# Optimization experiments

Hardware: AMD Instinct MI355X
Metric: run time of the kernel (lower is better)

## Reference

```python
import jax, jax.numpy as jnp
import numpy as np

B, L, D = 8, 1024, 1024  # L must equal D for the elementwise sqrt(K) divide to broadcast


def setup_inputs() -> dict:
    key = jax.random.key(0)
    ks = jax.random.split(key, 9)
    # Non-negative inputs/weights/biases so K = x @ Wk.T + bk >= 0 and sqrt(K) is finite.
    rc = jax.random.uniform(ks[0], (B, L, D), dtype=jnp.float32)
    ri = jax.random.uniform(ks[1], (B, L, D), dtype=jnp.float32)
    tc = jax.random.uniform(ks[2], (B, L, D), dtype=jnp.float32)
    scale = 0.02
    Wq = jax.random.uniform(ks[3], (D, D), dtype=jnp.float32) * scale
    Wk = jax.random.uniform(ks[4], (D, D), dtype=jnp.float32) * scale
    Wv = jax.random.uniform(ks[5], (D, D), dtype=jnp.float32) * scale
    bq = jax.random.uniform(ks[6], (D,), dtype=jnp.float32) * scale
    bk = jax.random.uniform(ks[7], (D,), dtype=jnp.float32) * scale
    bv = jax.random.uniform(ks[8], (D,), dtype=jnp.float32) * scale
    return {
        "reference_caption": rc,
        "reference_image": ri,
        "target_caption": tc,
        "Wq": Wq, "bq": bq,
        "Wk": Wk, "bk": bk,
        "Wv": Wv, "bv": bv,
    }


def reference(reference_caption, reference_image, target_caption, Wq, bq, Wk, bk, Wv, bv):
    # torch nn.Linear: y = x @ W.T + b
    Q = reference_caption @ Wq.T + bq          # [B, Lq, D]
    K = reference_image @ Wk.T + bk            # [B, Lk, D]
    V = reference_image @ Wv.T + bv            # [B, Lk, D]
    matmul_qk = jnp.einsum("bqd,bkd->bqk", Q, K)  # [B, Lq, Lk]
    # Faithful to source: elementwise divide by sqrt(K) tensor (broadcasts since Lq==Lk==D).
    scaled_logits = matmul_qk / jnp.sqrt(K)
    attention_weights = jax.nn.softmax(scaled_logits, axis=-1)
    output = jnp.einsum("bqk,bkd->bqd", attention_weights, V)
    return (output, attention_weights)
```

## Files before the change

### kernel.cpp

```cpp
#include <hip/hip_runtime.h>
#include <hip/hip_fp16.h>
#include <math.h>

typedef unsigned short u16;
typedef __attribute__((ext_vector_type(8))) _Float16 half8;
typedef __attribute__((ext_vector_type(4))) float f32x4;

#define ASLOT 4096
#define BSLOT 8192
#define SLOT  12288

__device__ __forceinline__ u16 f2h(float f){ __half h=__float2half(f); u16 r; __builtin_memcpy(&r,&h,2); return r; }
__device__ __forceinline__ float h2f(u16 u){ __half h; __builtin_memcpy(&h,&u,2); return __half2float(h); }

template<int ROWS, bool WRAP>
__device__ __forceinline__ void stage_tile(const u16* __restrict__ G, int rowbase, int ldg,
                                           int k0, u16* Ls, int tid){
#pragma unroll
    for (int p = 0; p < ROWS / 64; ++p){
        const int lin = tid + p * 256;
        const int row = lin >> 2;
        const int cg  = ((lin & 3) ^ ((row >> 1) & 3)) * 8;
        const int kk  = WRAP ? (k0 & 1023) : k0;
        const u16* g = G + (size_t)(rowbase + row) * ldg + (kk + cg);
        __builtin_amdgcn_global_load_lds(
            (__attribute__((address_space(1))) void*)g,
            (__attribute__((address_space(3))) void*)(Ls + (size_t)lin * 8), 16, 0, 0);
    }
}

template<int EPI, int BIASM, bool AWRAP, bool BWRAP>
__device__ __forceinline__ void gemm_core(
    const u16* __restrict__ A, const u16* __restrict__ B,
    const float* __restrict__ bias,
    float* __restrict__ of, u16* __restrict__ oh,
    int by, int bx, int lda, int ldb, int ldc, int K, u16* sh)
{
    const int tid  = threadIdx.x;
    const int lane = tid & 63, wv = tid >> 6;
    const int wr = (wv >> 1) * 64;
    const int wc = (wv & 1) * 128;
    const int row0 = by * 128, col0 = bx * 256;
    const int lr = lane & 15, hi = lane >> 4;
    const int co = (hi ^ ((lr >> 1) & 3)) * 8;

    f32x4 acc[4][8];
#pragma unroll
    for (int m = 0; m < 4; m++)
#pragma unroll
        for (int n = 0; n < 8; n++) acc[m][n] = (f32x4){0.f, 0.f, 0.f, 0.f};

    auto stage_set = [&](int buf, int k0){
        u16* s = sh + buf * SLOT;
        stage_tile<128, AWRAP>(A, row0, lda, k0, s, tid);
        stage_tile<256, BWRAP>(B, col0, ldb, k0, s + ASLOT, tid);
    };

    const int NIT = K >> 5;
    stage_set(0, 0);
    stage_set(1, 32);
    int bufs = 2, bufr = 0;
    for (int t = 0; t < NIT; ++t){
        if (t + 2 < NIT){ stage_set(bufs, (t + 2) << 5); bufs = (bufs + 1 == 3) ? 0 : bufs + 1; }
        const int rem = NIT - 1 - t;
        if (rem >= 2)      asm volatile("s_waitcnt vmcnt(12)" ::: "memory");
        else if (rem == 1) asm volatile("s_waitcnt vmcnt(6)" ::: "memory");
        else               asm volatile("s_waitcnt vmcnt(0)" ::: "memory");
        __builtin_amdgcn_s_barrier();
        __builtin_amdgcn_sched_barrier(0);

        const u16* s = sh + bufr * SLOT;
        bufr = (bufr + 1 == 3) ? 0 : bufr + 1;

        half8 a[4], b[8];
#pragma unroll
        for (int m = 0; m < 4; m++) a[m] = *(const half8*)&s[(wr + m * 16 + lr) * 32 + co];
#pragma unroll
        for (int n = 0; n < 8; n++) b[n] = *(const half8*)&s[ASLOT + (wc + n * 16 + lr) * 32 + co];
#pragma unroll
        for (int m = 0; m < 4; m++)
#pragma unroll
            for (int n = 0; n < 8; n++)
                acc[m][n] = __builtin_amdgcn_mfma_f32_16x16x32_f16(a[m], b[n], acc[m][n], 0, 0, 0);
        __builtin_amdgcn_sched_barrier(0);
        __builtin_amdgcn_s_barrier();
    }

#pragma unroll
    for (int m = 0; m < 4; m++) {
        const int rb = row0 + wr + m * 16 + hi * 4;
#pragma unroll
        for (int n = 0; n < 8; n++) {
            const int c = col0 + wc + n * 16 + lr;
            const float bc = (BIASM == 1) ? bias[c] : 0.f;
#pragma unroll
            for (int q = 0; q < 4; q++) {
                const int r = rb + q;
                float v = acc[m][n][q] + bc;
                if (BIASM == 2) v += bias[r];
                const size_t idx = (size_t)r * ldc + c;
                if (EPI == 0) of[idx] = v;
                else if (EPI == 1) oh[idx] = f2h(v);
                else { const u16 hh = f2h(v); oh[idx] = hh; oh[idx + 1024] = f2h(v - h2f(hh)); }
            }
        }
    }
}

__global__ __launch_bounds__(256, 2) void lin_qk_k(
    const u16* __restrict__ rc_h, const u16* __restrict__ ri_hl,
    const u16* __restrict__ Wq_h, const u16* __restrict__ Wk_h,
    const float* __restrict__ bq, const float* __restrict__ bk,
    u16* __restrict__ Q_h, u16* __restrict__ Kcat)
{
    __shared__ __align__(16) u16 sh[3 * SLOT];
    const int nwg = gridDim.x, chunk = nwg >> 3;
    const int swz = ((int)blockIdx.x & 7) * chunk + ((int)blockIdx.x >> 3);
    const int p = swz & 1, t = swz >> 1;
    if (p == 0) {
        gemm_core<1, 1, false, false>(rc_h, Wq_h, bq, nullptr, Q_h,
                                      t >> 2, t & 3, 1024, 1024, 1024, 1024, sh);
    } else {
        gemm_core<2, 1, false, true>(ri_hl, Wk_h, bk, nullptr, Kcat,
                                     t >> 2, t & 3, 2048, 1024, 2048, 2048, sh);
    }
}

__global__ __launch_bounds__(256, 2) void qkt_vt_k(
    const u16* __restrict__ Q_h, const u16* __restrict__ Kcat,
    const u16* __restrict__ ri_hl, const u16* __restrict__ Wv_h,
    const float* __restrict__ bv,
    float* __restrict__ wts, u16* __restrict__ Vt)
{
    __shared__ __align__(16) u16 sh[3 * SLOT];
    const int nwg = gridDim.x, chunk = nwg >> 3;
    const int swz = ((int)blockIdx.x & 7) * chunk + ((int)blockIdx.x >> 3);
    const int p = swz & 1, t = swz >> 1;
    if (p == 0) {
        const int z = t >> 5, rem = t & 31;
        gemm_core<0, 0, true, false>(Q_h + (size_t)z * 1048576, Kcat + (size_t)z * 1024 * 2048,
                                     nullptr, wts + (size_t)z * 1048576, nullptr,
                                     rem >> 2, rem & 3, 1024, 2048, 1024, 2048, sh);
    } else {
        gemm_core<1, 2, false, false>(Wv_h, ri_hl, bv, nullptr, Vt,
                                      t >> 5, t & 31, 1024, 2048, 8192, 1024, sh);
    }
}

__global__ __launch_bounds__(256, 2) void av_k(
    const u16* __restrict__ W_h, const u16* __restrict__ Vt, float* __restrict__ outp)
{
    __shared__ __align__(16) u16 sh[3 * SLOT];
    const int nwg = gridDim.x, chunk = nwg >> 3;
    const int wg = ((int)blockIdx.x & 7) * chunk + ((int)blockIdx.x >> 3);
    const int z = wg >> 5, rem = wg & 31;
    gemm_core<0, 0, false, false>(W_h + (size_t)z * 1048576, Vt + (size_t)z * 1024,
                                  nullptr, outp + (size_t)z * 1048576, nullptr,
                                  rem >> 2, rem & 3, 1024, 8192, 1024, 1024, sh);
}

__global__ __launch_bounds__(256)
void softmax_scale_k(float* __restrict__ W, const u16* __restrict__ Kcat, u16* __restrict__ Wh)
{
    const long row = blockIdx.x;
    float* p = W + (row << 10);
    const int tid = threadIdx.x;

    float4 v = ((const float4*)p)[tid];
    const ushort4 kh = ((const ushort4*)(Kcat + (row << 11)))[tid];
    const ushort4 kl = ((const ushort4*)(Kcat + (row << 11) + 1024))[tid];
    v.x *= rsqrtf(h2f(kh.x) + h2f(kl.x));
    v.y *= rsqrtf(h2f(kh.y) + h2f(kl.y));
    v.z *= rsqrtf(h2f(kh.z) + h2f(kl.z));
    v.w *= rsqrtf(h2f(kh.w) + h2f(kl.w));

    float m = fmaxf(fmaxf(v.x, v.y), fmaxf(v.z, v.w));
#pragma unroll
    for (int o = 32; o >= 1; o >>= 1) m = fmaxf(m, __shfl_xor(m, o));
    __shared__ float sm[4];
    const int wid = tid >> 6, lane = tid & 63;
    if (lane == 0) sm[wid] = m;
    __syncthreads();
    m = fmaxf(fmaxf(sm[0], sm[1]), fmaxf(sm[2], sm[3]));

    v.x = __expf(v.x - m); v.y = __expf(v.y - m);
    v.z = __expf(v.z - m); v.w = __expf(v.w - m);
    float s = v.x + v.y + v.z + v.w;
#pragma unroll
    for (int o = 32; o >= 1; o >>= 1) s += __shfl_xor(s, o);
    __shared__ float ss[4];
    if (lane == 0) ss[wid] = s;
    __syncthreads();
    s = ss[0] + ss[1] + ss[2] + ss[3];

    const float inv = 1.0f / s;
    v.x *= inv; v.y *= inv; v.z *= inv; v.w *= inv;
    ((float4*)p)[tid] = v;

    ushort4 ub;
    ub.x = f2h(v.x); ub.y = f2h(v.y); ub.z = f2h(v.z); ub.w = f2h(v.w);
    ((ushort4*)(Wh + (row << 10)))[tid] = ub;
}

__global__ __launch_bounds__(256)
void conv_split_k(const float4* __restrict__ x, u16* __restrict__ dst, int n4)
{
    const int i = blockIdx.x * 256 + threadIdx.x;
    if (i >= n4) return;
    const int row = i >> 8, c4 = i & 255;
    const float4 v = x[i];
    ushort4 hh, ll;
    hh.x = f2h(v.x); ll.x = f2h(v.x - h2f(hh.x));
    hh.y = f2h(v.y); ll.y = f2h(v.y - h2f(hh.y));
    hh.z = f2h(v.z); ll.z = f2h(v.z - h2f(hh.z));
    hh.w = f2h(v.w); ll.w = f2h(v.w - h2f(hh.w));
    ((ushort4*)(dst + (size_t)row * 2048))[c4] = hh;
    ((ushort4*)(dst + (size_t)row * 2048 + 1024))[c4] = ll;
}

__global__ __launch_bounds__(256)
void conv_plain4_k(const float4* __restrict__ x0, ushort4* __restrict__ y0,
                   const float4* __restrict__ x1, ushort4* __restrict__ y1,
                   const float4* __restrict__ x2, ushort4* __restrict__ y2,
                   const float4* __restrict__ x3, ushort4* __restrict__ y3)
{
    const long i = (long)blockIdx.x * 256 + threadIdx.x;
    const long n0 = 2097152, n1 = 262144;
    const float4* x; ushort4* y; long j;
    if (i < n0)            { x = x0; y = y0; j = i; }
    else if (i < n0 + n1)  { x = x1; y = y1; j = i - n0; }
    else if (i < n0 + 2*n1){ x = x2; y = y2; j = i - n0 - n1; }
    else                   { x = x3; y = y3; j = i - n0 - 2*n1; }
    const float4 v = x[j];
    ushort4 o;
    o.x = f2h(v.x); o.y = f2h(v.y); o.z = f2h(v.z); o.w = f2h(v.w);
    y[j] = o;
}

extern "C" void kernel_launch(void* const* d_in, const int* in_sizes, int n_in,
                              void* d_out, int out_size, void* d_ws, size_t ws_size,
                              hipStream_t stream)
{
    const float* rc = (const float*)d_in[0];
    const float* ri = (const float*)d_in[1];
    const float* Wq = (const float*)d_in[3];
    const float* bq = (const float*)d_in[4];
    const float* Wk = (const float*)d_in[5];
    const float* bk = (const float*)d_in[6];
    const float* Wv = (const float*)d_in[7];
    const float* bv = (const float*)d_in[8];

    const long M8 = 8192 * 1024L;
    const long M1 = 1024 * 1024L;

    u16* ws    = (u16*)d_ws;
    u16* ri_hl = ws;
    u16* rc_h  = ws + 2 * M8;
    u16* Kcat  = ws + 3 * M8;
    u16* Wq_h  = ws + 5 * M8;
    u16* Wk_h  = Wq_h + M1;
    u16* Wv_h  = Wk_h + M1;

    float* outp = (float*)d_out;
    float* wts  = outp + M8;
    u16*   Q_h  = (u16*)d_out;
    u16*   Vt   = rc_h;
    u16*   W_h  = ri_hl;

    conv_split_k<<<8192, 256, 0, stream>>>((const float4*)ri, ri_hl, (int)(M8 / 4));
    conv_plain4_k<<<11264, 256, 0, stream>>>(
        (const float4*)rc, (ushort4*)rc_h, (const float4*)Wq, (ushort4*)Wq_h,
        (const float4*)Wk, (ushort4*)Wk_h, (const float4*)Wv, (ushort4*)Wv_h);

    lin_qk_k<<<512, 256, 0, stream>>>(rc_h, ri_hl, Wq_h, Wk_h, bq, bk, Q_h, Kcat);

    qkt_vt_k<<<512, 256, 0, stream>>>(Q_h, Kcat, ri_hl, Wv_h, bv, wts, Vt);

    softmax_scale_k<<<8192, 256, 0, stream>>>(wts, Kcat, W_h);

    av_k<<<256, 256, 0, stream>>>(W_h, Vt, outp);
}
```

Measured before the change: 196.9 us.

## Replace GEMM core with 256x256 tile, 8-wave ping-pong pipelined kernel

```diff
diff --git a/kernel.cpp b/kernel.cpp
--- a/kernel.cpp
+++ b/kernel.cpp
@@ -6,31 +6,17 @@
 typedef __attribute__((ext_vector_type(8))) _Float16 half8;
 typedef __attribute__((ext_vector_type(4))) float f32x4;
 
-#define ASLOT 4096
-#define BSLOT 8192
-#define SLOT  12288
-
 __device__ __forceinline__ u16 f2h(float f){ __half h=__float2half(f); u16 r; __builtin_memcpy(&r,&h,2); return r; }
 __device__ __forceinline__ float h2f(u16 u){ __half h; __builtin_memcpy(&h,&u,2); return __half2float(h); }
 
-template<int ROWS, bool WRAP>
-__device__ __forceinline__ void stage_tile(const u16* __restrict__ G, int rowbase, int ldg,
-                                           int k0, u16* Ls, int tid){
-#pragma unroll
-    for (int p = 0; p < ROWS / 64; ++p){
-        const int lin = tid + p * 256;
-        const int row = lin >> 2;
-        const int cg  = ((lin & 3) ^ ((row >> 1) & 3)) * 8;
-        const int kk  = WRAP ? (k0 & 1023) : k0;
-        const u16* g = G + (size_t)(rowbase + row) * ldg + (kk + cg);
-        __builtin_amdgcn_global_load_lds(
-            (__attribute__((address_space(1))) void*)g,
-            (__attribute__((address_space(3))) void*)(Ls + (size_t)lin * 8), 16, 0, 0);
-    }
-}
-
-template<int EPI, int BIASM, bool AWRAP, bool BWRAP>
-__device__ __forceinline__ void gemm_core(
+#define SYNC1 do{ __builtin_amdgcn_sched_barrier(0); __builtin_amdgcn_s_barrier(); \
+    asm volatile("s_waitcnt lgkmcnt(0)" ::: "memory"); __builtin_amdgcn_sched_barrier(0); \
+    __builtin_amdgcn_s_setprio(1); }while(0)
+#define SYNC2 do{ __builtin_amdgcn_s_setprio(0); __builtin_amdgcn_sched_barrier(0); \
+    __builtin_amdgcn_s_barrier(); }while(0)
+
+template<int EPI, int BIASM, bool AWRAP>
+__device__ __forceinline__ void gemm8(
     const u16* __restrict__ A, const u16* __restrict__ B,
     const float* __restrict__ bias,
     float* __restrict__ of, u16* __restrict__ oh,
@@ -38,63 +24,113 @@
 {
     const int tid  = threadIdx.x;
     const int lane = tid & 63, wv = tid >> 6;
-    const int wr = (wv >> 1) * 64;
-    const int wc = (wv & 1) * 128;
-    const int row0 = by * 128, col0 = bx * 256;
+    const int wr = (wv >> 2) * 128;
+    const int wc = (wv & 3) * 64;
+    const int row0 = by * 256, col0 = bx * 256;
     const int lr = lane & 15, hi = lane >> 4;
-    const int co = (hi ^ ((lr >> 1) & 3)) * 8;
-
-    f32x4 acc[4][8];
-#pragma unroll
-    for (int m = 0; m < 4; m++)
-#pragma unroll
-        for (int n = 0; n < 8; n++) acc[m][n] = (f32x4){0.f, 0.f, 0.f, 0.f};
-
-    auto stage_set = [&](int buf, int k0){
-        u16* s = sh + buf * SLOT;
-        stage_tile<128, AWRAP>(A, row0, lda, k0, s, tid);
-        stage_tile<256, BWRAP>(B, col0, ldb, k0, s + ASLOT, tid);
+
+    f32x4 acc[8][4];
+#pragma unroll
+    for (int m = 0; m < 8; m++)
+#pragma unroll
+        for (int n = 0; n < 4; n++) acc[m][n] = (f32x4){0.f, 0.f, 0.f, 0.f};
+
+    auto STG = [&](int op, int kt, int half){
+        const u16* G = op ? B : A;
+        const int  ld = op ? ldb : lda;
+        const int  rb = (op ? col0 : row0) + half * 128;
+        int k0 = kt << 6;
+        if (AWRAP && op == 0) k0 &= 1023;
+        u16* dst = sh + ((kt & 1) << 15) + (op << 14) + (half << 13);
+#pragma unroll
+        for (int p = 0; p < 2; ++p){
+            const int lin = tid + p * 512;
+            const int r  = lin >> 3;
+            const int ch = (lin & 7) ^ (r & 7);
+            const u16* g = G + (size_t)(rb + r) * ld + k0 + ch * 8;
+            __builtin_amdgcn_global_load_lds(
+                (__attribute__((address_space(1))) void*)g,
+                (__attribute__((address_space(3))) void*)(dst + (size_t)lin * 8), 16, 0, 0);
+        }
     };
-
-    const int NIT = K >> 5;
-    stage_set(0, 0);
-    stage_set(1, 32);
-    int bufs = 2, bufr = 0;
-    for (int t = 0; t < NIT; ++t){
-        if (t + 2 < NIT){ stage_set(bufs, (t + 2) << 5); bufs = (bufs + 1 == 3) ? 0 : bufs + 1; }
-        const int rem = NIT - 1 - t;
-        if (rem >= 2)      asm volatile("s_waitcnt vmcnt(12)" ::: "memory");
-        else if (rem == 1) asm volatile("s_waitcnt vmcnt(6)" ::: "memory");
-        else               asm volatile("s_waitcnt vmcnt(0)" ::: "memory");
-        __builtin_amdgcn_s_barrier();
-        __builtin_amdgcn_sched_barrier(0);
-
-        const u16* s = sh + bufr * SLOT;
-        bufr = (bufr + 1 == 3) ? 0 : bufr + 1;
-
-        half8 a[4], b[8];
-#pragma unroll
-        for (int m = 0; m < 4; m++) a[m] = *(const half8*)&s[(wr + m * 16 + lr) * 32 + co];
-#pragma unroll
-        for (int n = 0; n < 8; n++) b[n] = *(const half8*)&s[ASLOT + (wc + n * 16 + lr) * 32 + co];
-#pragma unroll
-        for (int m = 0; m < 4; m++)
-#pragma unroll
-            for (int n = 0; n < 8; n++)
-                acc[m][n] = __builtin_amdgcn_mfma_f32_16x16x32_f16(a[m], b[n], acc[m][n], 0, 0, 0);
-        __builtin_amdgcn_sched_barrier(0);
-        __builtin_amdgcn_s_barrier();
+    auto LDA_ = [&](half8* a, int kt, int mh){
+        const u16* base = sh + ((kt & 1) << 15);
+#pragma unroll
+        for (int mi = 0; mi < 4; ++mi)
+#pragma unroll
+            for (int ks = 0; ks < 2; ++ks){
+                const int r = wr + (mh * 4 + mi) * 16 + lr;
+                a[mi * 2 + ks] = *(const half8*)&base[(size_t)r * 64 + (((hi + ks * 4) ^ (lr & 7)) * 8)];
+            }
+    };
+    auto LDB_ = [&](half8* b, int kt, int nh){
+        const u16* base = sh + ((kt & 1) << 15) + 16384;
+#pragma unroll
+        for (int ni = 0; ni < 2; ++ni)
+#pragma unroll
+            for (int ks = 0; ks < 2; ++ks){
+                const int r = wc + (nh * 2 + ni) * 16 + lr;
+                b[ni * 2 + ks] = *(const half8*)&base[(size_t)r * 64 + (((hi + ks * 4) ^ (lr & 7)) * 8)];
+            }
+    };
+    auto MM = [&](half8* a, half8* b, int mh, int nh){
+#pragma unroll
+        for (int mi = 0; mi < 4; ++mi)
+#pragma unroll
+            for (int ni = 0; ni < 2; ++ni)
+#pragma unroll
+                for (int ks = 0; ks < 2; ++ks)
+                    acc[mh * 4 + mi][nh * 2 + ni] = __builtin_amdgcn_mfma_f32_16x16x32_f16(
+                        a[mi * 2 + ks], b[ni * 2 + ks], acc[mh * 4 + mi][nh * 2 + ni], 0, 0, 0);
+    };
+
+    const int NKT = K >> 6, NIT = NKT >> 1;
+    STG(1, 0, 0); STG(1, 0, 1); STG(0, 0, 0); STG(0, 0, 1);
+    STG(1, 1, 0); STG(1, 1, 1);
+    asm volatile("s_waitcnt vmcnt(4)" ::: "memory");
+    __builtin_amdgcn_s_barrier();
+
+    half8 a[8], b0[4], b1[4];
+    for (int i = 0; i < NIT; ++i){
+        const int t0 = 2 * i, t1 = 2 * i + 1;
+        const bool more = (i + 1 < NIT);
+        LDA_(a, t0, 0); LDB_(b0, t0, 0);
+        STG(0, t1, 0);
+        SYNC1; MM(a, b0, 0, 0); SYNC2;
+        LDB_(b1, t0, 1);
+        STG(0, t1, 1);
+        SYNC1; MM(a, b1, 0, 1); SYNC2;
+        LDA_(a, t0, 1);
+        if (more) STG(1, t0 + 2, 0);
+        SYNC1; MM(a, b1, 1, 1); SYNC2;
+        if (more) STG(1, t0 + 2, 1);
+        if (more) asm volatile("s_waitcnt vmcnt(4)" ::: "memory");
+        else      asm volatile("s_waitcnt vmcnt(0)" ::: "memory");
+        SYNC1; MM(a, b0, 1, 0); SYNC2;
+        LDA_(a, t1, 0); LDB_(b0, t1, 0);
+        if (more) STG(0, t0 + 2, 0);
+        SYNC1; MM(a, b0, 0, 0); SYNC2;
+        LDB_(b1, t1, 1);
+        if (more) STG(0, t0 + 2, 1);
+        SYNC1; MM(a, b1, 0, 1); SYNC2;
+        LDA_(a, t1, 1);
+        if (more) STG(1, t1 + 2, 0);
+        SYNC1; MM(a, b1, 1, 1); SYNC2;
+        if (more) STG(1, t1 + 2, 1);
+        if (more) asm volatile("s_waitcnt vmcnt(4)" ::: "memory");
+        else      asm volatile("s_waitcnt vmcnt(0)" ::: "memory");
+        SYNC1; MM(a, b0, 1, 0); SYNC2;
     }
 
 #pragma unroll
-    for (int m = 0; m < 4; m++) {
+    for (int m = 0; m < 8; m++){
         const int rb = row0 + wr + m * 16 + hi * 4;
 #pragma unroll
-        for (int n = 0; n < 8; n++) {
+        for (int n = 0; n < 4; n++){
             const int c = col0 + wc + n * 16 + lr;
             const float bc = (BIASM == 1) ? bias[c] : 0.f;
 #pragma unroll
-            for (int q = 0; q < 4; q++) {
+            for (int q = 0; q < 4; q++){
                 const int r = rb + q;
                 float v = acc[m][n][q] + bc;
                 if (BIASM == 2) v += bias[r];
@@ -107,56 +143,56 @@
     }
 }
 
-__global__ __launch_bounds__(256, 2) void lin_qk_k(
+__global__ __launch_bounds__(512, 1) void lin_qk_k(
     const u16* __restrict__ rc_h, const u16* __restrict__ ri_hl,
     const u16* __restrict__ Wq_h, const u16* __restrict__ Wk_h,
     const float* __restrict__ bq, const float* __restrict__ bk,
     u16* __restrict__ Q_h, u16* __restrict__ Kcat)
 {
-    __shared__ __align__(16) u16 sh[3 * SLOT];
+    __shared__ __align__(16) u16 sh[65536];
     const int nwg = gridDim.x, chunk = nwg >> 3;
     const int swz = ((int)blockIdx.x & 7) * chunk + ((int)blockIdx.x >> 3);
     const int p = swz & 1, t = swz >> 1;
     if (p == 0) {
-        gemm_core<1, 1, false, false>(rc_h, Wq_h, bq, nullptr, Q_h,
-                                      t >> 2, t & 3, 1024, 1024, 1024, 1024, sh);
+        gemm8<1, 1, false>(rc_h, Wq_h, bq, nullptr, Q_h,
+                           t >> 2, t & 3, 1024, 1024, 1024, 1024, sh);
     } else {
-        gemm_core<2, 1, false, true>(ri_hl, Wk_h, bk, nullptr, Kcat,
-                                     t >> 2, t & 3, 2048, 1024, 2048, 2048, sh);
+        gemm8<2, 1, false>(ri_hl, Wk_h, bk, nullptr, Kcat,
+                           t >> 2, t & 3, 2048, 1024, 2048, 2048, sh);
     }
 }
 
-__global__ __launch_bounds__(256, 2) void qkt_vt_k(
+__global__ __launch_bounds__(512, 1) void qkt_vt_k(
     const u16* __restrict__ Q_h, const u16* __restrict__ Kcat,
     const u16* __restrict__ ri_hl, const u16* __restrict__ Wv_h,
     const float* __restrict__ bv,
     float* __restrict__ wts, u16* __restrict__ Vt)
 {
-    __shared__ __align__(16) u16 sh[3 * SLOT];
+    __shared__ __align__(16) u16 sh[65536];
     const int nwg = gridDim.x, chunk = nwg >> 3;
     const int swz = ((int)blockIdx.x & 7) * chunk + ((int)blockIdx.x >> 3);
     const int p = swz & 1, t = swz >> 1;
     if (p == 0) {
-        const int z = t >> 5, rem = t & 31;
-        gemm_core<0, 0, true, false>(Q_h + (size_t)z * 1048576, Kcat + (size_t)z * 1024 * 2048,
-                                     nullptr, wts + (size_t)z * 1048576, nullptr,
-                                     rem >> 2, rem & 3, 1024, 2048, 1024, 2048, sh);
+        const int z = t >> 4, rem = t & 15;
+        gemm8<0, 0, true>(Q_h + (size_t)z * 1048576, Kcat + (size_t)z * 2097152,
+                          nullptr, wts + (size_t)z * 1048576, nullptr,
+                          rem >> 2, rem & 3, 1024, 2048, 1024, 2048, sh);
     } else {
-        gemm_core<1, 2, false, false>(Wv_h, ri_hl, bv, nullptr, Vt,
-                                      t >> 5, t & 31, 1024, 2048, 8192, 1024, sh);
+        gemm8<1, 2, false>(Wv_h, ri_hl, bv, nullptr, Vt,
+                           t >> 5, t & 31, 1024, 2048, 8192, 1024, sh);
     }
 }
 
-__global__ __launch_bounds__(256, 2) void av_k(
+__global__ __launch_bounds__(512, 1) void av_k(
     const u16* __restrict__ W_h, const u16* __restrict__ Vt, float* __restrict__ outp)
 {
-    __shared__ __align__(16) u16 sh[3 * SLOT];
+    __shared__ __align__(16) u16 sh[65536];
     const int nwg = gridDim.x, chunk = nwg >> 3;
     const int wg = ((int)blockIdx.x & 7) * chunk + ((int)blockIdx.x >> 3);
-    const int z = wg >> 5, rem = wg & 31;
-    gemm_core<0, 0, false, false>(W_h + (size_t)z * 1048576, Vt + (size_t)z * 1024,
-                                  nullptr, outp + (size_t)z * 1048576, nullptr,
-                                  rem >> 2, rem & 3, 1024, 8192, 1024, 1024, sh);
+    const int z = wg >> 4, rem = wg & 15;
+    gemm8<0, 0, false>(W_h + (size_t)z * 1048576, Vt + (size_t)z * 1024,
+                       nullptr, outp + (size_t)z * 1048576, nullptr,
+                       rem >> 2, rem & 3, 1024, 8192, 1024, 1024, sh);
 }
 
 __global__ __launch_bounds__(256)
@@ -272,11 +308,11 @@
         (const float4*)rc, (ushort4*)rc_h, (const float4*)Wq, (ushort4*)Wq_h,
         (const float4*)Wk, (ushort4*)Wk_h, (const float4*)Wv, (ushort4*)Wv_h);
 
-    lin_qk_k<<<512, 256, 0, stream>>>(rc_h, ri_hl, Wq_h, Wk_h, bq, bk, Q_h, Kcat);
-
-    qkt_vt_k<<<512, 256, 0, stream>>>(Q_h, Kcat, ri_hl, Wv_h, bv, wts, Vt);
+    lin_qk_k<<<256, 512, 0, stream>>>(rc_h, ri_hl, Wq_h, Wk_h, bq, bk, Q_h, Kcat);
+
+    qkt_vt_k<<<256, 512, 0, stream>>>(Q_h, Kcat, ri_hl, Wv_h, bv, wts, Vt);
 
     softmax_scale_k<<<8192, 256, 0, stream>>>(wts, Kcat, W_h);
 
-    av_k<<<256, 256, 0, stream>>>(W_h, Vt, outp);
-}
+    av_k<<<128, 512, 0, stream>>>(W_h, Vt, outp);
+}
```

After: 203.9 us. +3.6%, slower.
